# Kernel optimization log

Measured on AMD Instinct MI355X. Metric: run time of the kernel, lower is better.

## Reference

```python
import jax, jax.numpy as jnp
import numpy as np

B, H, S, D = 1, 16, 2048, 64
G, HK = 8, 2              # num_head_groups, head_kernel_size
QK, KK = 6, 11            # query_kernel_size, key_kernel_size
EPS = 1e-5


def setup_inputs() -> dict:
    key = jax.random.key(0)
    ks = jax.random.split(key, 6)
    q = jax.random.normal(ks[0], (B, H, S, D), jnp.float32)
    k = jax.random.normal(ks[1], (B, H, S, D), jnp.float32)
    v = jax.random.normal(ks[2], (B, H, S, D), jnp.float32)
    # depthwise conv weight [C_out=H, C_in/groups=1, QK, KK]: identity at center + noise
    conv_w = 0.02 * jax.random.normal(ks[3], (H, 1, QK, KK), jnp.float32)
    conv_w = conv_w.at[:, 0, QK // 2, KK // 2].add(1.0)
    conv_b = 0.01 * jax.random.normal(ks[4], (H,), jnp.float32)
    # head mixing weights [G, HK, HK]: identity init + noise
    head_mix = jnp.broadcast_to(jnp.eye(HK, dtype=jnp.float32), (G, HK, HK)) \
        + 0.1 * jax.random.normal(ks[5], (G, HK, HK), jnp.float32)
    ln_gamma = jnp.ones((D,), jnp.float32)
    ln_beta = jnp.zeros((D,), jnp.float32)
    return {"q": q, "k": k, "v": v, "conv_w": conv_w, "conv_b": conv_b,
            "head_mix": head_mix, "ln_gamma": ln_gamma, "ln_beta": ln_beta}


def _mta_forward(q, k, v, conv_w, conv_b, head_mix, ln_gamma, ln_beta):
    b, h, s, d = q.shape
    scale = 1.0 / np.sqrt(d).astype(np.float32)
    scores = jnp.einsum('bhsd,bhkd->bhsk', q, k) * scale          # [B,H,S,S]
    mask = jnp.triu(jnp.ones((s, s), dtype=bool), 1)              # strict upper = future
    # key-query convolution with double masking (paper eq. 4)
    masked = jnp.where(mask, 0.0, scores)
    # torch padding='same' for even kernel 6: left=2, right=3; for 11: (5,5)
    conv = jax.lax.conv_general_dilated(
        masked, conv_w, window_strides=(1, 1),
        padding=[(2, 3), (5, 5)],
        dimension_numbers=('NCHW', 'OIHW', 'NCHW'),
        feature_group_count=h)
    conv = conv + conv_b[None, :, None, None]
    final = jnp.where(mask, -1e9, conv)
    w = jax.nn.softmax(final, axis=-1)
    # post-softmax head mixing within groups of HK heads
    wg = w.reshape(b, G, HK, s, s)
    mixed = jnp.einsum('bgisk,gij->bgjsk', wg, head_mix).reshape(b, h, s, s)
    out = jnp.einsum('bhsk,bhkd->bhsd', mixed, v)                 # [B,H,S,D]
    # LayerNorm over head_dim (torch uses biased variance)
    mu = jnp.mean(out, axis=-1, keepdims=True)
    var = jnp.mean(jnp.square(out - mu), axis=-1, keepdims=True)
    return (out - mu) * jax.lax.rsqrt(var + EPS) * ln_gamma + ln_beta


def reference(q, k, v, conv_w, conv_b, head_mix, ln_gamma, ln_beta):
    return _mta_forward(q, k, v, conv_w, conv_b, head_mix, ln_gamma, ln_beta)
```

## Files before the change

kernel.cpp:

```cpp
#include <hip/hip_runtime.h>
#include <math.h>

#define SS 2048
#define QP 72
#define KP 72
#define VP 72
#define SFP 88
#define PP 72

typedef __attribute__((ext_vector_type(8))) short s8v;
typedef __attribute__((ext_vector_type(8))) _Float16 h8v;
typedef __attribute__((ext_vector_type(4))) float f4v;

__device__ __forceinline__ unsigned short f2b(float x) {
    union { float f; unsigned u; } v; v.f = x;
    unsigned r = v.u + 0x7FFFu + ((v.u >> 16) & 1u);
    return (unsigned short)(r >> 16);
}

__device__ __forceinline__ unsigned long long pack4(float4 v) {
    return (unsigned long long)f2b(v.x) | ((unsigned long long)f2b(v.y) << 16)
         | ((unsigned long long)f2b(v.z) << 32) | ((unsigned long long)f2b(v.w) << 48);
}

__global__ __launch_bounds__(512, 2)
void mta_v9(const float* __restrict__ Q, const float* __restrict__ K,
            const float* __restrict__ V, const float* __restrict__ CW,
            const float* __restrict__ CB, const float* __restrict__ MIX,
            const float* __restrict__ GAM, const float* __restrict__ BET,
            float* __restrict__ OUT)
{
    __shared__ __align__(16) unsigned short sQ[96 * QP];
    __shared__ __align__(16) unsigned short sK[2][160 * KP];
    __shared__ __align__(16) unsigned short sVt[2][128 * VP];
    __shared__ __align__(16) _Float16 sSf[96 * SFP];
    __shared__ __align__(16) unsigned short sP[64 * PP];
    __shared__ float sResc[2][32];
    __shared__ float sL[2][32];
    __shared__ float sW2[2][66];
    __shared__ float sB2[2];

    const int tid = threadIdx.x;
    const int g = blockIdx.x & 7;
    const int u = blockIdx.x >> 3;

    const int wv = tid >> 6, lane = tid & 63;
    const int lrow = lane & 15;
    const int lk8 = (lane >> 4) << 3;
    const int crow4 = (lane >> 4) << 2;

    const int i_pv = wv >> 2, j_pv = (wv >> 1) & 1, kh = wv & 1;
    const int hC = wv >> 1, mtw = wv & 1;

    for (int idx = tid; idx < 132; idx += 512) {
        int h = idx / 66, w = idx - h * 66;
        sW2[h][w] = CW[(2 * g + h) * 66 + w];
    }
    if (tid < 2) sB2[tid] = CB[2 * g + tid];
    const float mixc = MIX[g * 4 + i_pv * 2 + j_pv];
    __syncthreads();

    h8v tf[6];
    float biasC = 0.f;
    if (wv < 4) {
        biasC = sB2[hC];
#pragma unroll
        for (int i = 0; i < 6; ++i)
#pragma unroll
            for (int e = 0; e < 8; ++e) {
                int d = lk8 + e - lrow;
                tf[i][e] = (d >= 0 && d <= 10) ? (_Float16)sW2[hC][i * 11 + d] : (_Float16)0.f;
            }
    }

    const float4* Q4 = (const float4*)Q;
    const float4* K4 = (const float4*)K;
    const float4* V4 = (const float4*)V;

    for (int ti = 0; ti < 2; ++ti) {
        const int tile = ti ? u : (63 - u);
        const int q0 = tile << 5;
        __syncthreads();

        for (int idx = tid; idx < 1536; idx += 512) {
            int h = idx / 768, rem = idx - h * 768;
            int e = rem >> 4, d4 = rem & 15;
            int r = q0 - 2 + e;
            float4 val = make_float4(0.f, 0.f, 0.f, 0.f);
            if (r >= 0 && r < SS) val = Q4[((2 * g + h) * SS + r) * 16 + d4];
            *(unsigned long long*)&sQ[(h * 48 + e) * QP + (d4 << 2)] = pack4(val);
        }
        for (int idx = tid; idx < 2560; idx += 512) {
            int h = idx / 1280, rem = idx - h * 1280;
            int e = rem >> 4, d4 = rem & 15;
            int c = -5 + e;
            float4 val = make_float4(0.f, 0.f, 0.f, 0.f);
            if (e < 74 && c >= 0 && c < SS) val = K4[((2 * g + h) * SS + c) * 16 + d4];
            *(unsigned long long*)&sK[0][(h * 80 + e) * KP + (d4 << 2)] = pack4(val);
        }
        for (int idx = tid; idx < 2048; idx += 512) {
            int h = idx >> 10, d4 = (idx >> 6) & 15, kk = idx & 63;
            float4 val = V4[((2 * g + h) * SS + kk) * 16 + d4];
            int d = d4 << 2;
            sVt[0][(h * 64 + d + 0) * VP + kk] = f2b(val.x);
            sVt[0][(h * 64 + d + 1) * VP + kk] = f2b(val.y);
            sVt[0][(h * 64 + d + 2) * VP + kk] = f2b(val.z);
            sVt[0][(h * 64 + d + 3) * VP + kk] = f2b(val.w);
        }

        f4v acc[2][4];
#pragma unroll
        for (int mt = 0; mt < 2; ++mt)
#pragma unroll
            for (int nt = 0; nt < 4; ++nt) acc[mt][nt] = f4v{0.f, 0.f, 0.f, 0.f};
        float m_run[4], l_run[4];
#pragma unroll
        for (int r = 0; r < 4; ++r) { m_run[r] = -INFINITY; l_run[r] = 0.f; }
        int cur = 0;

        __syncthreads();

        const int iters = (tile >> 1) + 1;
        for (int it = 0; it < iters; ++it) {
            const int k0 = it << 6;
            const bool pf = (it + 1) < iters;
            const int k0n = (it + 1) << 6;
            const int nxt = cur ^ 1;

            for (int job = wv; job < 30; job += 8) {
                int h = job / 15, r15 = job - h * 15;
                int mt = r15 / 5, nt = r15 - mt * 5;
                const unsigned short* ap = &sQ[(h * 48 + mt * 16 + lrow) * QP + lk8];
                const unsigned short* bp = &sK[cur][(h * 80 + nt * 16 + lrow) * KP + lk8];
                f4v c = f4v{0.f, 0.f, 0.f, 0.f};
                c = __builtin_amdgcn_mfma_f32_16x16x32_bf16(*(const s8v*)ap,
                                                            *(const s8v*)bp, c, 0, 0, 0);
                c = __builtin_amdgcn_mfma_f32_16x16x32_bf16(*(const s8v*)(ap + 32),
                                                            *(const s8v*)(bp + 32), c, 0, 0, 0);
                int col = nt * 16 + lrow;
                int cab = k0 - 5 + col;
                int rbase = mt * 16 + crow4;
#pragma unroll
                for (int r = 0; r < 4; ++r)
                    sSf[(h * 48 + rbase + r) * SFP + col] =
                        (_Float16)((cab <= q0 - 2 + rbase + r) ? c[r] * 0.125f : 0.f);
            }
            __syncthreads();

            if (wv < 4) {
                f4v cc[4];
#pragma unroll
                for (int ct = 0; ct < 4; ++ct) {
                    f4v c = f4v{0.f, 0.f, 0.f, 0.f};
#pragma unroll
                    for (int i = 0; i < 6; ++i) {
                        h8v a = *(const h8v*)&sSf[(hC * 48 + mtw * 16 + i + lrow) * SFP + ct * 16 + lk8];
                        c = __builtin_amdgcn_mfma_f32_16x16x32_f16(a, tf[i], c, 0, 0, 0);
                    }
                    cc[ct] = c;
                }
                const int rowa0 = q0 + mtw * 16 + crow4;
#pragma unroll
                for (int r = 0; r < 4; ++r) {
                    float tm = -INFINITY;
#pragma unroll
                    for (int ct = 0; ct < 4; ++ct) {
                        float v = cc[ct][r] + biasC;
                        int ca = k0 + ct * 16 + lrow;
                        if (ca > rowa0 + r) v = -1e9f;
                        cc[ct][r] = v;
                        tm = fmaxf(tm, v);
                    }
                    tm = fmaxf(tm, __shfl_xor(tm, 1));
                    tm = fmaxf(tm, __shfl_xor(tm, 2));
                    tm = fmaxf(tm, __shfl_xor(tm, 4));
                    tm = fmaxf(tm, __shfl_xor(tm, 8));
                    float mnew = fmaxf(m_run[r], tm);
                    float resc = __expf(m_run[r] - mnew);
                    m_run[r] = mnew;
                    float ps = 0.f;
#pragma unroll
                    for (int ct = 0; ct < 4; ++ct) {
                        float p = __expf(cc[ct][r] - mnew);
                        cc[ct][r] = p;
                        ps += p;
                    }
                    ps += __shfl_xor(ps, 1);
                    ps += __shfl_xor(ps, 2);
                    ps += __shfl_xor(ps, 4);
                    ps += __shfl_xor(ps, 8);
                    l_run[r] = l_run[r] * resc + ps;
                    if (lrow == 0) sResc[hC][mtw * 16 + crow4 + r] = resc;
                }
#pragma unroll
                for (int ct = 0; ct < 4; ++ct)
#pragma unroll
                    for (int r = 0; r < 4; ++r)
                        sP[(hC * 32 + mtw * 16 + crow4 + r) * PP + ct * 16 + lrow] = f2b(cc[ct][r]);
            } else if (pf) {
                const int stid = ((wv - 4) << 6) + lane;
                float4 kreg[10], vreg[8];
#pragma unroll
                for (int n = 0; n < 10; ++n) {
                    int idx = stid + (n << 8);
                    int h = idx / 1280, rem = idx - h * 1280;
                    int e = rem >> 4, d4 = rem & 15;
                    int c = k0n - 5 + e;
                    kreg[n] = make_float4(0.f, 0.f, 0.f, 0.f);
                    if (e < 74 && c >= 0 && c < SS)
                        kreg[n] = K4[((2 * g + h) * SS + c) * 16 + d4];
                }
#pragma unroll
                for (int n = 0; n < 8; ++n) {
                    int idx = stid + (n << 8);
                    int h = idx >> 10, d4 = (idx >> 6) & 15, kk = idx & 63;
                    vreg[n] = V4[((2 * g + h) * SS + k0n + kk) * 16 + d4];
                }
#pragma unroll
                for (int n = 0; n < 10; ++n) {
                    int idx = stid + (n << 8);
                    int h = idx / 1280, rem = idx - h * 1280;
                    int e = rem >> 4, d4 = rem & 15;
                    *(unsigned long long*)&sK[nxt][(h * 80 + e) * KP + (d4 << 2)] = pack4(kreg[n]);
                }
#pragma unroll
                for (int n = 0; n < 8; ++n) {
                    int idx = stid + (n << 8);
                    int h = idx >> 10, d4 = (idx >> 6) & 15, kk = idx & 63;
                    int d = d4 << 2;
                    sVt[nxt][(h * 64 + d + 0) * VP + kk] = f2b(vreg[n].x);
                    sVt[nxt][(h * 64 + d + 1) * VP + kk] = f2b(vreg[n].y);
                    sVt[nxt][(h * 64 + d + 2) * VP + kk] = f2b(vreg[n].z);
                    sVt[nxt][(h * 64 + d + 3) * VP + kk] = f2b(vreg[n].w);
                }
            }
            __syncthreads();

            {
#pragma unroll
                for (int mt = 0; mt < 2; ++mt)
#pragma unroll
                    for (int r = 0; r < 4; ++r) {
                        float f = sResc[i_pv][mt * 16 + crow4 + r];
#pragma unroll
                        for (int nt = 0; nt < 4; ++nt) acc[mt][nt][r] *= f;
                    }
#pragma unroll
                for (int mt = 0; mt < 2; ++mt) {
                    s8v a = *(const s8v*)&sP[(i_pv * 32 + mt * 16 + lrow) * PP + (kh << 5) + lk8];
#pragma unroll
                    for (int nt = 0; nt < 4; ++nt) {
                        s8v b = *(const s8v*)&sVt[cur][(j_pv * 64 + nt * 16 + lrow) * VP + (kh << 5) + lk8];
                        acc[mt][nt] = __builtin_amdgcn_mfma_f32_16x16x32_bf16(a, b, acc[mt][nt], 0, 0, 0);
                    }
                }
            }
            cur = nxt;
        }

        if (wv < 4 && lrow == 0) {
#pragma unroll
            for (int r = 0; r < 4; ++r) sL[hC][mtw * 16 + crow4 + r] = l_run[r];
        }
        __syncthreads();

        float* sO = (float*)&sK[0][0];
#pragma unroll
        for (int st = 0; st < 4; ++st) {
            if (i_pv == (st >> 1) && kh == (st & 1)) {
#pragma unroll
                for (int mt = 0; mt < 2; ++mt)
#pragma unroll
                    for (int r = 0; r < 4; ++r) {
                        int row = mt * 16 + crow4 + r;
                        float cc = mixc / sL[i_pv][row];
#pragma unroll
                        for (int nt = 0; nt < 4; ++nt) {
                            int col = nt * 16 + lrow;
                            float val = acc[mt][nt][r] * cc;
                            if (st == 0) sO[(j_pv * 32 + row) * 68 + col] = val;
                            else         sO[(j_pv * 32 + row) * 68 + col] += val;
                        }
                    }
            }
            __syncthreads();
        }

        {
            const float4* G4 = (const float4*)GAM;
            const float4* B4 = (const float4*)BET;
#pragma unroll
            for (int itl = 0; itl < 2; ++itl) {
                int pidx = tid + (itl << 9);
                int d4 = pidx & 15, rowj = pidx >> 4;
                int j = rowj >> 5, qq = rowj & 31;
                float4 o = *(const float4*)&sO[rowj * 68 + (d4 << 2)];
                float s1 = o.x + o.y + o.z + o.w;
                float s2 = o.x * o.x + o.y * o.y + o.z * o.z + o.w * o.w;
#pragma unroll
                for (int off = 1; off < 16; off <<= 1) {
                    s1 += __shfl_xor(s1, off);
                    s2 += __shfl_xor(s2, off);
                }
                float mean = s1 * (1.f / 64.f);
                float var = s2 * (1.f / 64.f) - mean * mean;
                float rs = rsqrtf(var + 1e-5f);
                float4 gm = G4[d4], bt = B4[d4];
                float4 ov;
                ov.x = (o.x - mean) * rs * gm.x + bt.x;
                ov.y = (o.y - mean) * rs * gm.y + bt.y;
                ov.z = (o.z - mean) * rs * gm.z + bt.z;
                ov.w = (o.w - mean) * rs * gm.w + bt.w;
                *(float4*)&OUT[(((2 * g + j) * SS + q0 + qq) << 6) + (d4 << 2)] = ov;
            }
        }
    }
}

extern "C" void kernel_launch(void* const* d_in, const int* in_sizes, int n_in,
                              void* d_out, int out_size, void* d_ws, size_t ws_size,
                              hipStream_t stream) {
    const float* q = (const float*)d_in[0];
    const float* k = (const float*)d_in[1];
    const float* v = (const float*)d_in[2];
    const float* cw = (const float*)d_in[3];
    const float* cb = (const float*)d_in[4];
    const float* mix = (const float*)d_in[5];
    const float* gam = (const float*)d_in[6];
    const float* bet = (const float*)d_in[7];
    float* out = (float*)d_out;

    dim3 grid(8 * 32);
    dim3 block(512);
    hipLaunchKernelGGL(mta_v9, grid, block, 0, stream,
                       q, k, v, cw, cb, mix, gam, bet, out);
}
```

Before: 125.3 us.

## Double block to 1024 threads and split PV, prefetch and epilogue across 16 waves

Grows the workgroup from 8 to 16 wavefronts. The P·V accumulation is split further across waves by output-column half, cutting per-wave accumulators. The K/V prefetch for the next tile is spread over 12 waves instead of 4, and LayerNorm finishes in a single pass. It also raises instruction priority around the convolution MFMAs. The goal is more latency hiding and parallelism per CU, at the cost of a tighter register budget and more barrier participants.

```diff
diff --git a/kernel.cpp b/kernel.cpp
--- a/kernel.cpp
+++ b/kernel.cpp
@@ -23,12 +23,13 @@
          | ((unsigned long long)f2b(v.z) << 32) | ((unsigned long long)f2b(v.w) << 48);
 }
 
-__global__ __launch_bounds__(512, 2)
-void mta_v9(const float* __restrict__ Q, const float* __restrict__ K,
-            const float* __restrict__ V, const float* __restrict__ CW,
-            const float* __restrict__ CB, const float* __restrict__ MIX,
-            const float* __restrict__ GAM, const float* __restrict__ BET,
-            float* __restrict__ OUT)
+__global__ __launch_bounds__(1024, 4)
+__attribute__((amdgpu_waves_per_eu(4, 4)))
+void mta_v10(const float* __restrict__ Q, const float* __restrict__ K,
+             const float* __restrict__ V, const float* __restrict__ CW,
+             const float* __restrict__ CB, const float* __restrict__ MIX,
+             const float* __restrict__ GAM, const float* __restrict__ BET,
+             float* __restrict__ OUT)
 {
     __shared__ __align__(16) unsigned short sQ[96 * QP];
     __shared__ __align__(16) unsigned short sK[2][160 * KP];
@@ -49,10 +50,10 @@
     const int lk8 = (lane >> 4) << 3;
     const int crow4 = (lane >> 4) << 2;
 
-    const int i_pv = wv >> 2, j_pv = (wv >> 1) & 1, kh = wv & 1;
+    const int i_pv = (wv >> 3) & 1, j_pv = (wv >> 2) & 1, kh = (wv >> 1) & 1, nh = wv & 1;
     const int hC = wv >> 1, mtw = wv & 1;
 
-    for (int idx = tid; idx < 132; idx += 512) {
+    for (int idx = tid; idx < 132; idx += 1024) {
         int h = idx / 66, w = idx - h * 66;
         sW2[h][w] = CW[(2 * g + h) * 66 + w];
     }
@@ -82,7 +83,7 @@
         const int q0 = tile << 5;
         __syncthreads();
 
-        for (int idx = tid; idx < 1536; idx += 512) {
+        for (int idx = tid; idx < 1536; idx += 1024) {
             int h = idx / 768, rem = idx - h * 768;
             int e = rem >> 4, d4 = rem & 15;
             int r = q0 - 2 + e;
@@ -90,7 +91,7 @@
             if (r >= 0 && r < SS) val = Q4[((2 * g + h) * SS + r) * 16 + d4];
             *(unsigned long long*)&sQ[(h * 48 + e) * QP + (d4 << 2)] = pack4(val);
         }
-        for (int idx = tid; idx < 2560; idx += 512) {
+        for (int idx = tid; idx < 2560; idx += 1024) {
             int h = idx / 1280, rem = idx - h * 1280;
             int e = rem >> 4, d4 = rem & 15;
             int c = -5 + e;
@@ -98,7 +99,7 @@
             if (e < 74 && c >= 0 && c < SS) val = K4[((2 * g + h) * SS + c) * 16 + d4];
             *(unsigned long long*)&sK[0][(h * 80 + e) * KP + (d4 << 2)] = pack4(val);
         }
-        for (int idx = tid; idx < 2048; idx += 512) {
+        for (int idx = tid; idx < 2048; idx += 1024) {
             int h = idx >> 10, d4 = (idx >> 6) & 15, kk = idx & 63;
             float4 val = V4[((2 * g + h) * SS + kk) * 16 + d4];
             int d = d4 << 2;
@@ -108,11 +109,11 @@
             sVt[0][(h * 64 + d + 3) * VP + kk] = f2b(val.w);
         }
 
-        f4v acc[2][4];
+        f4v acc[2][2];
 #pragma unroll
         for (int mt = 0; mt < 2; ++mt)
 #pragma unroll
-            for (int nt = 0; nt < 4; ++nt) acc[mt][nt] = f4v{0.f, 0.f, 0.f, 0.f};
+            for (int n2 = 0; n2 < 2; ++n2) acc[mt][n2] = f4v{0.f, 0.f, 0.f, 0.f};
         float m_run[4], l_run[4];
 #pragma unroll
         for (int r = 0; r < 4; ++r) { m_run[r] = -INFINITY; l_run[r] = 0.f; }
@@ -127,7 +128,7 @@
             const int k0n = (it + 1) << 6;
             const int nxt = cur ^ 1;
 
-            for (int job = wv; job < 30; job += 8) {
+            for (int job = wv; job < 30; job += 16) {
                 int h = job / 15, r15 = job - h * 15;
                 int mt = r15 / 5, nt = r15 - mt * 5;
                 const unsigned short* ap = &sQ[(h * 48 + mt * 16 + lrow) * QP + lk8];
@@ -149,6 +150,7 @@
 
             if (wv < 4) {
                 f4v cc[4];
+                __builtin_amdgcn_s_setprio(1);
 #pragma unroll
                 for (int ct = 0; ct < 4; ++ct) {
                     f4v c = f4v{0.f, 0.f, 0.f, 0.f};
@@ -159,6 +161,7 @@
                     }
                     cc[ct] = c;
                 }
+                __builtin_amdgcn_s_setprio(0);
                 const int rowa0 = q0 + mtw * 16 + crow4;
 #pragma unroll
                 for (int r = 0; r < 4; ++r) {
@@ -199,59 +202,67 @@
                         sP[(hC * 32 + mtw * 16 + crow4 + r) * PP + ct * 16 + lrow] = f2b(cc[ct][r]);
             } else if (pf) {
                 const int stid = ((wv - 4) << 6) + lane;
-                float4 kreg[10], vreg[8];
-#pragma unroll
-                for (int n = 0; n < 10; ++n) {
-                    int idx = stid + (n << 8);
-                    int h = idx / 1280, rem = idx - h * 1280;
-                    int e = rem >> 4, d4 = rem & 15;
-                    int c = k0n - 5 + e;
+                float4 kreg[4], vreg[3];
+#pragma unroll
+                for (int n = 0; n < 4; ++n) {
+                    int idx = stid + n * 768;
                     kreg[n] = make_float4(0.f, 0.f, 0.f, 0.f);
-                    if (e < 74 && c >= 0 && c < SS)
-                        kreg[n] = K4[((2 * g + h) * SS + c) * 16 + d4];
-                }
-#pragma unroll
-                for (int n = 0; n < 8; ++n) {
-                    int idx = stid + (n << 8);
-                    int h = idx >> 10, d4 = (idx >> 6) & 15, kk = idx & 63;
-                    vreg[n] = V4[((2 * g + h) * SS + k0n + kk) * 16 + d4];
-                }
-#pragma unroll
-                for (int n = 0; n < 10; ++n) {
-                    int idx = stid + (n << 8);
-                    int h = idx / 1280, rem = idx - h * 1280;
-                    int e = rem >> 4, d4 = rem & 15;
-                    *(unsigned long long*)&sK[nxt][(h * 80 + e) * KP + (d4 << 2)] = pack4(kreg[n]);
-                }
-#pragma unroll
-                for (int n = 0; n < 8; ++n) {
-                    int idx = stid + (n << 8);
-                    int h = idx >> 10, d4 = (idx >> 6) & 15, kk = idx & 63;
-                    int d = d4 << 2;
-                    sVt[nxt][(h * 64 + d + 0) * VP + kk] = f2b(vreg[n].x);
-                    sVt[nxt][(h * 64 + d + 1) * VP + kk] = f2b(vreg[n].y);
-                    sVt[nxt][(h * 64 + d + 2) * VP + kk] = f2b(vreg[n].z);
-                    sVt[nxt][(h * 64 + d + 3) * VP + kk] = f2b(vreg[n].w);
+                    if (idx < 2560) {
+                        int h = idx / 1280, rem = idx - h * 1280;
+                        int e = rem >> 4, d4 = rem & 15;
+                        int c = k0n - 5 + e;
+                        if (e < 74 && c >= 0 && c < SS)
+                            kreg[n] = K4[((2 * g + h) * SS + c) * 16 + d4];
+                    }
+                }
+#pragma unroll
+                for (int n = 0; n < 3; ++n) {
+                    int idx = stid + n * 768;
+                    vreg[n] = make_float4(0.f, 0.f, 0.f, 0.f);
+                    if (idx < 2048) {
+                        int h = idx >> 10, d4 = (idx >> 6) & 15, kk = idx & 63;
+                        vreg[n] = V4[((2 * g + h) * SS + k0n + kk) * 16 + d4];
+                    }
+                }
+#pragma unroll
+                for (int n = 0; n < 4; ++n) {
+                    int idx = stid + n * 768;
+                    if (idx < 2560) {
+                        int h = idx / 1280, rem = idx - h * 1280;
+                        int e = rem >> 4, d4 = rem & 15;
+                        *(unsigned long long*)&sK[nxt][(h * 80 + e) * KP + (d4 << 2)] = pack4(kreg[n]);
+                    }
+                }
+#pragma unroll
+                for (int n = 0; n < 3; ++n) {
+                    int idx = stid + n * 768;
+                    if (idx < 2048) {
+                        int h = idx >> 10, d4 = (idx >> 6) & 15, kk = idx & 63;
+                        int d = d4 << 2;
+                        sVt[nxt][(h * 64 + d + 0) * VP + kk] = f2b(vreg[n].x);
+                        sVt[nxt][(h * 64 + d + 1) * VP + kk] = f2b(vreg[n].y);
+                        sVt[nxt][(h * 64 + d + 2) * VP + kk] = f2b(vreg[n].z);
+                        sVt[nxt][(h * 64 + d + 3) * VP + kk] = f2b(vreg[n].w);
+                    }
                 }
             }
             __syncthreads();
 
             {
 #pragma unroll
-                for (int mt = 0; mt < 2; ++mt)
+                for (int mt = 0; mt < 2; ++mt) {
 #pragma unroll
                     for (int r = 0; r < 4; ++r) {
                         float f = sResc[i_pv][mt * 16 + crow4 + r];
-#pragma unroll
-                        for (int nt = 0; nt < 4; ++nt) acc[mt][nt][r] *= f;
-                    }
-#pragma unroll
-                for (int mt = 0; mt < 2; ++mt) {
+                        acc[mt][0][r] *= f;
+                        acc[mt][1][r] *= f;
+                    }
                     s8v a = *(const s8v*)&sP[(i_pv * 32 + mt * 16 + lrow) * PP + (kh << 5) + lk8];
 #pragma unroll
-                    for (int nt = 0; nt < 4; ++nt) {
+                    for (int n2 = 0; n2 < 2; ++n2) {
+                        int nt = nh * 2 + n2;
                         s8v b = *(const s8v*)&sVt[cur][(j_pv * 64 + nt * 16 + lrow) * VP + (kh << 5) + lk8];
-                        acc[mt][nt] = __builtin_amdgcn_mfma_f32_16x16x32_bf16(a, b, acc[mt][nt], 0, 0, 0);
+                        acc[mt][n2] = __builtin_amdgcn_mfma_f32_16x16x32_bf16(a, b, acc[mt][n2], 0, 0, 0);
                     }
                 }
             }
@@ -273,11 +284,11 @@
 #pragma unroll
                     for (int r = 0; r < 4; ++r) {
                         int row = mt * 16 + crow4 + r;
-                        float cc = mixc / sL[i_pv][row];
-#pragma unroll
-                        for (int nt = 0; nt < 4; ++nt) {
-                            int col = nt * 16 + lrow;
-                            float val = acc[mt][nt][r] * cc;
+                        float cc2 = mixc / sL[i_pv][row];
+#pragma unroll
+                        for (int n2 = 0; n2 < 2; ++n2) {
+                            int col = (nh * 2 + n2) * 16 + lrow;
+                            float val = acc[mt][n2][r] * cc2;
                             if (st == 0) sO[(j_pv * 32 + row) * 68 + col] = val;
                             else         sO[(j_pv * 32 + row) * 68 + col] += val;
                         }
@@ -289,30 +300,26 @@
         {
             const float4* G4 = (const float4*)GAM;
             const float4* B4 = (const float4*)BET;
-#pragma unroll
-            for (int itl = 0; itl < 2; ++itl) {
-                int pidx = tid + (itl << 9);
-                int d4 = pidx & 15, rowj = pidx >> 4;
-                int j = rowj >> 5, qq = rowj & 31;
-                float4 o = *(const float4*)&sO[rowj * 68 + (d4 << 2)];
-                float s1 = o.x + o.y + o.z + o.w;
-                float s2 = o.x * o.x + o.y * o.y + o.z * o.z + o.w * o.w;
-#pragma unroll
-                for (int off = 1; off < 16; off <<= 1) {
-                    s1 += __shfl_xor(s1, off);
-                    s2 += __shfl_xor(s2, off);
-                }
-                float mean = s1 * (1.f / 64.f);
-                float var = s2 * (1.f / 64.f) - mean * mean;
-                float rs = rsqrtf(var + 1e-5f);
-                float4 gm = G4[d4], bt = B4[d4];
-                float4 ov;
-                ov.x = (o.x - mean) * rs * gm.x + bt.x;
-                ov.y = (o.y - mean) * rs * gm.y + bt.y;
-                ov.z = (o.z - mean) * rs * gm.z + bt.z;
-                ov.w = (o.w - mean) * rs * gm.w + bt.w;
-                *(float4*)&OUT[(((2 * g + j) * SS + q0 + qq) << 6) + (d4 << 2)] = ov;
-            }
+            int d4 = tid & 15, rowj = tid >> 4;
+            int j = rowj >> 5, qq = rowj & 31;
+            float4 o = *(const float4*)&sO[rowj * 68 + (d4 << 2)];
+            float s1 = o.x + o.y + o.z + o.w;
+            float s2 = o.x * o.x + o.y * o.y + o.z * o.z + o.w * o.w;
+#pragma unroll
+            for (int off = 1; off < 16; off <<= 1) {
+                s1 += __shfl_xor(s1, off);
+                s2 += __shfl_xor(s2, off);
+            }
+            float mean = s1 * (1.f / 64.f);
+            float var = s2 * (1.f / 64.f) - mean * mean;
+            float rs = rsqrtf(var + 1e-5f);
+            float4 gm = G4[d4], bt = B4[d4];
+            float4 ov;
+            ov.x = (o.x - mean) * rs * gm.x + bt.x;
+            ov.y = (o.y - mean) * rs * gm.y + bt.y;
+            ov.z = (o.z - mean) * rs * gm.z + bt.z;
+            ov.w = (o.w - mean) * rs * gm.w + bt.w;
+            *(float4*)&OUT[(((2 * g + j) * SS + q0 + qq) << 6) + (d4 << 2)] = ov;
         }
     }
 }
@@ -331,7 +338,7 @@
     float* out = (float*)d_out;
 
     dim3 grid(8 * 32);
-    dim3 block(512);
-    hipLaunchKernelGGL(mta_v9, grid, block, 0, stream,
+    dim3 block(1024);
+    hipLaunchKernelGGL(mta_v10, grid, block, 0, stream,
                        q, k, v, cw, cb, mix, gam, bet, out);
 }
```

After: 135.6 us. +8.2%, slower.

## Switch attention operands to fp16 and transpose conv MFMA for per-lane row softmax

Applied to the files above, without the earlier changes.

Converts Q, K, V and P staging from software bf16 rounding to fp16 using packed hardware conversions, and uses fp16 MFMAs throughout. The conv MFMA operands are swapped so each lane owns one query row, which lets the softmax reduce with two cross-group shuffles instead of four per row, and lets P be written with packed 8-byte stores. The bias is folded into the accumulator init, wave priority is raised around the conv MFMAs, and integer divisions become compares. fp16 narrows the exponent range compared with bf16, which may matter for large activations.

```diff
diff --git a/kernel.cpp b/kernel.cpp
--- a/kernel.cpp
+++ b/kernel.cpp
@@ -8,33 +8,29 @@
 #define SFP 88
 #define PP 72
 
-typedef __attribute__((ext_vector_type(8))) short s8v;
 typedef __attribute__((ext_vector_type(8))) _Float16 h8v;
+typedef __attribute__((ext_vector_type(2))) __fp16 p2v;
 typedef __attribute__((ext_vector_type(4))) float f4v;
 
-__device__ __forceinline__ unsigned short f2b(float x) {
-    union { float f; unsigned u; } v; v.f = x;
-    unsigned r = v.u + 0x7FFFu + ((v.u >> 16) & 1u);
-    return (unsigned short)(r >> 16);
+__device__ __forceinline__ unsigned long long pack4h(float4 v) {
+    union { p2v h[2]; unsigned long long u; } t;
+    t.h[0] = __builtin_amdgcn_cvt_pkrtz(v.x, v.y);
+    t.h[1] = __builtin_amdgcn_cvt_pkrtz(v.z, v.w);
+    return t.u;
 }
 
-__device__ __forceinline__ unsigned long long pack4(float4 v) {
-    return (unsigned long long)f2b(v.x) | ((unsigned long long)f2b(v.y) << 16)
-         | ((unsigned long long)f2b(v.z) << 32) | ((unsigned long long)f2b(v.w) << 48);
-}
-
 __global__ __launch_bounds__(512, 2)
-void mta_v9(const float* __restrict__ Q, const float* __restrict__ K,
-            const float* __restrict__ V, const float* __restrict__ CW,
-            const float* __restrict__ CB, const float* __restrict__ MIX,
-            const float* __restrict__ GAM, const float* __restrict__ BET,
-            float* __restrict__ OUT)
+void mta_v11(const float* __restrict__ Q, const float* __restrict__ K,
+             const float* __restrict__ V, const float* __restrict__ CW,
+             const float* __restrict__ CB, const float* __restrict__ MIX,
+             const float* __restrict__ GAM, const float* __restrict__ BET,
+             float* __restrict__ OUT)
 {
-    __shared__ __align__(16) unsigned short sQ[96 * QP];
-    __shared__ __align__(16) unsigned short sK[2][160 * KP];
-    __shared__ __align__(16) unsigned short sVt[2][128 * VP];
+    __shared__ __align__(16) _Float16 sQ[96 * QP];
+    __shared__ __align__(16) _Float16 sK[2][160 * KP];
+    __shared__ __align__(16) _Float16 sVt[2][128 * VP];
     __shared__ __align__(16) _Float16 sSf[96 * SFP];
-    __shared__ __align__(16) unsigned short sP[64 * PP];
+    __shared__ __align__(16) _Float16 sP[64 * PP];
     __shared__ float sResc[2][32];
     __shared__ float sL[2][32];
     __shared__ float sW2[2][66];
@@ -53,8 +49,8 @@
     const int hC = wv >> 1, mtw = wv & 1;
 
     for (int idx = tid; idx < 132; idx += 512) {
-        int h = idx / 66, w = idx - h * 66;
-        sW2[h][w] = CW[(2 * g + h) * 66 + w];
+        int h = idx >= 66;
+        sW2[h][idx - (h ? 66 : 0)] = CW[(2 * g + h) * 66 + (idx - (h ? 66 : 0))];
     }
     if (tid < 2) sB2[tid] = CB[2 * g + tid];
     const float mixc = MIX[g * 4 + i_pv * 2 + j_pv];
@@ -83,29 +79,31 @@
         __syncthreads();
 
         for (int idx = tid; idx < 1536; idx += 512) {
-            int h = idx / 768, rem = idx - h * 768;
+            int h = idx >= 768;
+            int rem = idx - (h ? 768 : 0);
             int e = rem >> 4, d4 = rem & 15;
             int r = q0 - 2 + e;
             float4 val = make_float4(0.f, 0.f, 0.f, 0.f);
             if (r >= 0 && r < SS) val = Q4[((2 * g + h) * SS + r) * 16 + d4];
-            *(unsigned long long*)&sQ[(h * 48 + e) * QP + (d4 << 2)] = pack4(val);
+            *(unsigned long long*)&sQ[(h * 48 + e) * QP + (d4 << 2)] = pack4h(val);
         }
         for (int idx = tid; idx < 2560; idx += 512) {
-            int h = idx / 1280, rem = idx - h * 1280;
+            int h = idx >= 1280;
+            int rem = idx - (h ? 1280 : 0);
             int e = rem >> 4, d4 = rem & 15;
             int c = -5 + e;
             float4 val = make_float4(0.f, 0.f, 0.f, 0.f);
             if (e < 74 && c >= 0 && c < SS) val = K4[((2 * g + h) * SS + c) * 16 + d4];
-            *(unsigned long long*)&sK[0][(h * 80 + e) * KP + (d4 << 2)] = pack4(val);
+            *(unsigned long long*)&sK[0][(h * 80 + e) * KP + (d4 << 2)] = pack4h(val);
         }
         for (int idx = tid; idx < 2048; idx += 512) {
             int h = idx >> 10, d4 = (idx >> 6) & 15, kk = idx & 63;
             float4 val = V4[((2 * g + h) * SS + kk) * 16 + d4];
             int d = d4 << 2;
-            sVt[0][(h * 64 + d + 0) * VP + kk] = f2b(val.x);
-            sVt[0][(h * 64 + d + 1) * VP + kk] = f2b(val.y);
-            sVt[0][(h * 64 + d + 2) * VP + kk] = f2b(val.z);
-            sVt[0][(h * 64 + d + 3) * VP + kk] = f2b(val.w);
+            sVt[0][(h * 64 + d + 0) * VP + kk] = (_Float16)val.x;
+            sVt[0][(h * 64 + d + 1) * VP + kk] = (_Float16)val.y;
+            sVt[0][(h * 64 + d + 2) * VP + kk] = (_Float16)val.z;
+            sVt[0][(h * 64 + d + 3) * VP + kk] = (_Float16)val.w;
         }
 
         f4v acc[2][4];
@@ -113,9 +111,7 @@
         for (int mt = 0; mt < 2; ++mt)
 #pragma unroll
             for (int nt = 0; nt < 4; ++nt) acc[mt][nt] = f4v{0.f, 0.f, 0.f, 0.f};
-        float m_run[4], l_run[4];
-#pragma unroll
-        for (int r = 0; r < 4; ++r) { m_run[r] = -INFINITY; l_run[r] = 0.f; }
+        float m_run = -INFINITY, l_run = 0.f;
         int cur = 0;
 
         __syncthreads();
@@ -127,83 +123,91 @@
             const int k0n = (it + 1) << 6;
             const int nxt = cur ^ 1;
 
-            for (int job = wv; job < 30; job += 8) {
-                int h = job / 15, r15 = job - h * 15;
-                int mt = r15 / 5, nt = r15 - mt * 5;
-                const unsigned short* ap = &sQ[(h * 48 + mt * 16 + lrow) * QP + lk8];
-                const unsigned short* bp = &sK[cur][(h * 80 + nt * 16 + lrow) * KP + lk8];
-                f4v c = f4v{0.f, 0.f, 0.f, 0.f};
-                c = __builtin_amdgcn_mfma_f32_16x16x32_bf16(*(const s8v*)ap,
-                                                            *(const s8v*)bp, c, 0, 0, 0);
-                c = __builtin_amdgcn_mfma_f32_16x16x32_bf16(*(const s8v*)(ap + 32),
-                                                            *(const s8v*)(bp + 32), c, 0, 0, 0);
-                int col = nt * 16 + lrow;
-                int cab = k0 - 5 + col;
-                int rbase = mt * 16 + crow4;
-#pragma unroll
-                for (int r = 0; r < 4; ++r)
-                    sSf[(h * 48 + rbase + r) * SFP + col] =
-                        (_Float16)((cab <= q0 - 2 + rbase + r) ? c[r] * 0.125f : 0.f);
+#pragma unroll
+            for (int jj = 0; jj < 4; ++jj) {
+                int job = wv + (jj << 3);
+                if (job < 30) {
+                    int h = job >= 15;
+                    int r15 = job - (h ? 15 : 0);
+                    int mt = (r15 >= 10) ? 2 : ((r15 >= 5) ? 1 : 0);
+                    int nt = r15 - 5 * mt;
+                    const _Float16* ap = &sQ[(h * 48 + mt * 16 + lrow) * QP + lk8];
+                    const _Float16* bp = &sK[cur][(h * 80 + nt * 16 + lrow) * KP + lk8];
+                    f4v c = f4v{0.f, 0.f, 0.f, 0.f};
+                    c = __builtin_amdgcn_mfma_f32_16x16x32_f16(*(const h8v*)ap,
+                                                               *(const h8v*)bp, c, 0, 0, 0);
+                    c = __builtin_amdgcn_mfma_f32_16x16x32_f16(*(const h8v*)(ap + 32),
+                                                               *(const h8v*)(bp + 32), c, 0, 0, 0);
+                    int col = nt * 16 + lrow;
+                    int cab = k0 - 5 + col;
+                    int rbase = mt * 16 + crow4;
+#pragma unroll
+                    for (int r = 0; r < 4; ++r)
+                        sSf[(h * 48 + rbase + r) * SFP + col] =
+                            (_Float16)((cab <= q0 - 2 + rbase + r) ? c[r] * 0.125f : 0.f);
+                }
             }
             __syncthreads();
 
             if (wv < 4) {
                 f4v cc[4];
+                __builtin_amdgcn_s_setprio(1);
 #pragma unroll
                 for (int ct = 0; ct < 4; ++ct) {
-                    f4v c = f4v{0.f, 0.f, 0.f, 0.f};
+                    f4v c = f4v{biasC, biasC, biasC, biasC};
 #pragma unroll
                     for (int i = 0; i < 6; ++i) {
-                        h8v a = *(const h8v*)&sSf[(hC * 48 + mtw * 16 + i + lrow) * SFP + ct * 16 + lk8];
-                        c = __builtin_amdgcn_mfma_f32_16x16x32_f16(a, tf[i], c, 0, 0, 0);
+                        h8v b = *(const h8v*)&sSf[(hC * 48 + mtw * 16 + i + lrow) * SFP + ct * 16 + lk8];
+                        c = __builtin_amdgcn_mfma_f32_16x16x32_f16(tf[i], b, c, 0, 0, 0);
                     }
                     cc[ct] = c;
                 }
-                const int rowa0 = q0 + mtw * 16 + crow4;
-#pragma unroll
-                for (int r = 0; r < 4; ++r) {
-                    float tm = -INFINITY;
-#pragma unroll
-                    for (int ct = 0; ct < 4; ++ct) {
-                        float v = cc[ct][r] + biasC;
-                        int ca = k0 + ct * 16 + lrow;
-                        if (ca > rowa0 + r) v = -1e9f;
+                __builtin_amdgcn_s_setprio(0);
+                const int qrow = q0 + mtw * 16 + lrow;
+                float tm = -INFINITY;
+#pragma unroll
+                for (int ct = 0; ct < 4; ++ct)
+#pragma unroll
+                    for (int r = 0; r < 4; ++r) {
+                        int ca = k0 + ct * 16 + crow4 + r;
+                        float v = cc[ct][r];
+                        if (ca > qrow) v = -1e9f;
                         cc[ct][r] = v;
                         tm = fmaxf(tm, v);
                     }
-                    tm = fmaxf(tm, __shfl_xor(tm, 1));
-                    tm = fmaxf(tm, __shfl_xor(tm, 2));
-                    tm = fmaxf(tm, __shfl_xor(tm, 4));
-                    tm = fmaxf(tm, __shfl_xor(tm, 8));
-                    float mnew = fmaxf(m_run[r], tm);
-                    float resc = __expf(m_run[r] - mnew);
-                    m_run[r] = mnew;
-                    float ps = 0.f;
-#pragma unroll
-                    for (int ct = 0; ct < 4; ++ct) {
+                tm = fmaxf(tm, __shfl_xor(tm, 16));
+                tm = fmaxf(tm, __shfl_xor(tm, 32));
+                float mnew = fmaxf(m_run, tm);
+                float resc = __expf(m_run - mnew);
+                m_run = mnew;
+                float ps = 0.f;
+#pragma unroll
+                for (int ct = 0; ct < 4; ++ct)
+#pragma unroll
+                    for (int r = 0; r < 4; ++r) {
                         float p = __expf(cc[ct][r] - mnew);
                         cc[ct][r] = p;
                         ps += p;
                     }
-                    ps += __shfl_xor(ps, 1);
-                    ps += __shfl_xor(ps, 2);
-                    ps += __shfl_xor(ps, 4);
-                    ps += __shfl_xor(ps, 8);
-                    l_run[r] = l_run[r] * resc + ps;
-                    if (lrow == 0) sResc[hC][mtw * 16 + crow4 + r] = resc;
-                }
-#pragma unroll
-                for (int ct = 0; ct < 4; ++ct)
-#pragma unroll
-                    for (int r = 0; r < 4; ++r)
-                        sP[(hC * 32 + mtw * 16 + crow4 + r) * PP + ct * 16 + lrow] = f2b(cc[ct][r]);
+                ps += __shfl_xor(ps, 16);
+                ps += __shfl_xor(ps, 32);
+                l_run = l_run * resc + ps;
+                if ((lane >> 4) == 0) sResc[hC][mtw * 16 + lrow] = resc;
+#pragma unroll
+                for (int ct = 0; ct < 4; ++ct) {
+                    union { p2v h[2]; unsigned long long u; } t;
+                    t.h[0] = __builtin_amdgcn_cvt_pkrtz(cc[ct][0], cc[ct][1]);
+                    t.h[1] = __builtin_amdgcn_cvt_pkrtz(cc[ct][2], cc[ct][3]);
+                    *(unsigned long long*)&sP[(hC * 32 + mtw * 16 + lrow) * PP + ct * 16 + crow4] = t.u;
+                }
             } else if (pf) {
                 const int stid = ((wv - 4) << 6) + lane;
                 float4 kreg[10], vreg[8];
 #pragma unroll
                 for (int n = 0; n < 10; ++n) {
                     int idx = stid + (n << 8);
-                    int h = idx / 1280, rem = idx - h * 1280;
+                    int h = idx >= 1280;
+                    int rem = idx - (h ? 1280 : 0);
                     int e = rem >> 4, d4 = rem & 15;
                     int c = k0n - 5 + e;
                     kreg[n] = make_float4(0.f, 0.f, 0.f, 0.f);
@@ -219,19 +223,20 @@
 #pragma unroll
                 for (int n = 0; n < 10; ++n) {
                     int idx = stid + (n << 8);
-                    int h = idx / 1280, rem = idx - h * 1280;
+                    int h = idx >= 1280;
+                    int rem = idx - (h ? 1280 : 0);
                     int e = rem >> 4, d4 = rem & 15;
-                    *(unsigned long long*)&sK[nxt][(h * 80 + e) * KP + (d4 << 2)] = pack4(kreg[n]);
+                    *(unsigned long long*)&sK[nxt][(h * 80 + e) * KP + (d4 << 2)] = pack4h(kreg[n]);
                 }
 #pragma unroll
                 for (int n = 0; n < 8; ++n) {
                     int idx = stid + (n << 8);
                     int h = idx >> 10, d4 = (idx >> 6) & 15, kk = idx & 63;
                     int d = d4 << 2;
-                    sVt[nxt][(h * 64 + d + 0) * VP + kk] = f2b(vreg[n].x);
-                    sVt[nxt][(h * 64 + d + 1) * VP + kk] = f2b(vreg[n].y);
-                    sVt[nxt][(h * 64 + d + 2) * VP + kk] = f2b(vreg[n].z);
-                    sVt[nxt][(h * 64 + d + 3) * VP + kk] = f2b(vreg[n].w);
+                    sVt[nxt][(h * 64 + d + 0) * VP + kk] = (_Float16)vreg[n].x;
+                    sVt[nxt][(h * 64 + d + 1) * VP + kk] = (_Float16)vreg[n].y;
+                    sVt[nxt][(h * 64 + d + 2) * VP + kk] = (_Float16)vreg[n].z;
+                    sVt[nxt][(h * 64 + d + 3) * VP + kk] = (_Float16)vreg[n].w;
                 }
             }
             __syncthreads();
@@ -247,21 +252,18 @@
                     }
 #pragma unroll
                 for (int mt = 0; mt < 2; ++mt) {
-                    s8v a = *(const s8v*)&sP[(i_pv * 32 + mt * 16 + lrow) * PP + (kh << 5) + lk8];
+                    h8v a = *(const h8v*)&sP[(i_pv * 32 + mt * 16 + lrow) * PP + (kh << 5) + lk8];
 #pragma unroll
                     for (int nt = 0; nt < 4; ++nt) {
-                        s8v b = *(const s8v*)&sVt[cur][(j_pv * 64 + nt * 16 + lrow) * VP + (kh << 5) + lk8];
-                        acc[mt][nt] = __builtin_amdgcn_mfma_f32_16x16x32_bf16(a, b, acc[mt][nt], 0, 0, 0);
+                        h8v b = *(const h8v*)&sVt[cur][(j_pv * 64 + nt * 16 + lrow) * VP + (kh << 5) + lk8];
+                        acc[mt][nt] = __builtin_amdgcn_mfma_f32_16x16x32_f16(a, b, acc[mt][nt], 0, 0, 0);
                     }
                 }
             }
             cur = nxt;
         }
 
-        if (wv < 4 && lrow == 0) {
-#pragma unroll
-            for (int r = 0; r < 4; ++r) sL[hC][mtw * 16 + crow4 + r] = l_run[r];
-        }
+        if (wv < 4 && (lane >> 4) == 0) sL[hC][mtw * 16 + lrow] = l_run;
         __syncthreads();
 
         float* sO = (float*)&sK[0][0];
@@ -273,11 +275,11 @@
 #pragma unroll
                     for (int r = 0; r < 4; ++r) {
                         int row = mt * 16 + crow4 + r;
-                        float cc = mixc / sL[i_pv][row];
+                        float cc2 = mixc / sL[i_pv][row];
 #pragma unroll
                         for (int nt = 0; nt < 4; ++nt) {
                             int col = nt * 16 + lrow;
-                            float val = acc[mt][nt][r] * cc;
+                            float val = acc[mt][nt][r] * cc2;
                             if (st == 0) sO[(j_pv * 32 + row) * 68 + col] = val;
                             else         sO[(j_pv * 32 + row) * 68 + col] += val;
                         }
@@ -332,6 +334,6 @@
 
     dim3 grid(8 * 32);
     dim3 block(512);
-    hipLaunchKernelGGL(mta_v9, grid, block, 0, stream,
+    hipLaunchKernelGGL(mta_v11, grid, block, 0, stream,
                        q, k, v, cw, cb, mix, gam, bet, out);
 }
```

New measurement: 105.3 us. 15.9% less time.
